# Performance work log

Hardware: AMD Instinct MI355X
Metric: run time of the kernel (lower is better)

Reference implementation:

```python
import jax, jax.numpy as jnp
import numpy as np

NUM_HEADING_BIN = 12
NUM_SIZE_CLUSTER = 8
BS = 524288
# KITTI-style mean box sizes (l, w, h) for 8 size clusters
G_MEAN_SIZE_ARR = np.array([
    [3.88, 1.63, 1.53], [0.84, 0.66, 1.76], [1.76, 0.60, 1.74], [16.17, 2.58, 3.23],
    [3.90, 1.60, 1.56], [1.73, 0.58, 1.37], [0.91, 0.48, 1.78], [2.06, 1.86, 1.66]],
    dtype=np.float32)


def setup_inputs() -> dict:
    key = jax.random.key(0)
    ks = jax.random.split(key, 13)
    f = lambda k, s: jax.random.normal(k, s, dtype=jnp.float32)
    return {
        "center": f(ks[0], (BS, 3)),
        "center_label": f(ks[1], (BS, 3)),
        "stage1_center": f(ks[2], (BS, 3)),
        "heading_scores": f(ks[3], (BS, 12)),
        "heading_residuals_normalized": f(ks[4], (BS, 12)),
        "heading_residuals": f(ks[5], (BS, 12)),
        "heading_class_label": jax.random.randint(ks[6], (BS,), 0, 12, dtype=jnp.int64),
        "heading_residuals_label": f(ks[7], (BS,)),
        "size_scores": f(ks[8], (BS, 8)),
        "size_residuals_normalized": f(ks[9], (BS, 8, 3)),
        "size_residuals": f(ks[10], (BS, 8, 3)),
        "size_class_label": jax.random.randint(ks[11], (BS,), 0, 8, dtype=jnp.int64),
        "size_residuals_label": f(ks[12], (BS, 3)),
    }


def _huber(err, delta):
    a = jnp.abs(err)
    q = jnp.minimum(a, delta)
    return jnp.mean(0.5 * q * q + delta * (a - q))


_SX = jnp.array([1, 1, -1, -1, 1, 1, -1, -1], dtype=jnp.float32)
_SY = jnp.array([1, 1, 1, 1, -1, -1, -1, -1], dtype=jnp.float32)
_SZ = jnp.array([1, -1, -1, 1, 1, -1, -1, 1], dtype=jnp.float32)


def _corners3d(centers, headings, sizes):
    # centers (bs,3), headings (bs,), sizes (bs,3) [l,w,h] -> (bs,8,3)
    l, w, h = sizes[:, 0:1], sizes[:, 1:2], sizes[:, 2:3]
    x = 0.5 * l * _SX  # (bs,8)
    y = 0.5 * h * _SY
    z = 0.5 * w * _SZ
    c = jnp.cos(headings)[:, None]
    s = jnp.sin(headings)[:, None]
    xr = c * x + s * z   # rotation about y-axis
    zr = -s * x + c * z
    return jnp.stack([xr, y, zr], axis=-1) + centers[:, None, :]


def reference(center, center_label, stage1_center, heading_scores,
              heading_residuals_normalized, heading_residuals, heading_class_label,
              heading_residuals_label, size_scores, size_residuals_normalized,
              size_residuals, size_class_label, size_residuals_label):
    corner_loss_weight, box_loss_weight = 10.0, 1.0
    mean_sizes = jnp.asarray(G_MEAN_SIZE_ARR)  # (8,3)
    hcls = heading_class_label.astype(jnp.int32)
    scls = size_class_label.astype(jnp.int32)

    center_loss = _huber(jnp.linalg.norm(center - center_label, axis=1), 2.0)
    stage1_center_loss = _huber(jnp.linalg.norm(center - stage1_center, axis=1), 1.0)

    h_logp = jax.nn.log_softmax(heading_scores, axis=1)
    heading_class_loss = -jnp.mean(jnp.take_along_axis(h_logp, hcls[:, None], axis=1))
    s_logp = jax.nn.log_softmax(size_scores, axis=1)
    size_class_loss = -jnp.mean(jnp.take_along_axis(s_logp, scls[:, None], axis=1))

    # heading residual loss (one-hot sum == gather at class index)
    hres_label_norm = heading_residuals_label / (np.pi / NUM_HEADING_BIN)
    hres_pred = jnp.take_along_axis(heading_residuals_normalized, hcls[:, None], axis=1)[:, 0]
    heading_res_loss = _huber(hres_pred - hres_label_norm, 1.0)

    # size residual loss
    sres_pred = jnp.take_along_axis(size_residuals_normalized, scls[:, None, None], axis=1)[:, 0]  # (bs,3)
    mean_size_label = mean_sizes[scls]  # (bs,3)
    sres_label_norm = size_residuals_label / mean_size_label
    size_res_loss = _huber(jnp.linalg.norm(sres_label_norm - sres_pred, axis=1), 1.0)

    # corner loss: gt_mask one-hot sum over (NH,NS) grid == gather (hcls, scls) box
    bin_centers = jnp.arange(NUM_HEADING_BIN, dtype=jnp.float32) * (2.0 * np.pi / NUM_HEADING_BIN)
    heading_pred = jnp.take_along_axis(heading_residuals, hcls[:, None], axis=1)[:, 0] + bin_centers[hcls]
    size_pred = mean_size_label + jnp.take_along_axis(size_residuals, scls[:, None, None], axis=1)[:, 0]
    corners_pred = _corners3d(center, heading_pred, size_pred)  # (bs,8,3)

    heading_label = heading_residuals_label + bin_centers[hcls]
    size_label = mean_size_label + size_residuals_label
    corners_gt = _corners3d(center_label, heading_label, size_label)
    corners_gt_flip = _corners3d(center_label, heading_label + np.pi, size_label)
    corners_dist = jnp.minimum(jnp.linalg.norm(corners_pred - corners_gt, axis=-1),
                               jnp.linalg.norm(corners_pred - corners_gt_flip, axis=-1))
    corners_loss = _huber(corners_dist, 1.0)

    total_loss = box_loss_weight * (center_loss + heading_class_loss + size_class_loss
                                    + heading_res_loss * 20.0 + size_res_loss * 20.0
                                    + stage1_center_loss + corner_loss_weight * corners_loss)
    return total_loss
```

## Files before the change

### kernel.cpp

```cpp
#include <hip/hip_runtime.h>
#include <math.h>


constexpr int BS_N  = 524288;
constexpr int NBLK  = 2048;

__constant__ float G_MEAN[8][3] = {
    {3.88f, 1.63f, 1.53f}, {0.84f, 0.66f, 1.76f}, {1.76f, 0.60f, 1.74f},
    {16.17f, 2.58f, 3.23f}, {3.90f, 1.60f, 1.56f}, {1.73f, 0.58f, 1.37f},
    {0.91f, 0.48f, 1.78f}, {2.06f, 1.86f, 1.66f}
};

__device__ __forceinline__ float huber_pos(float a, float delta) {
    return (a <= delta) ? 0.5f * a * a : delta * (a - 0.5f * delta);
}
__device__ __forceinline__ float huber_norm2(float d2, float delta) {
    return (d2 <= delta * delta) ? 0.5f * d2
                                 : delta * (sqrtf(d2) - 0.5f * delta);
}

__global__ __launch_bounds__(256) void bbox_partial(
    const float* __restrict__ center,
    const float* __restrict__ center_label,
    const float* __restrict__ stage1_center,
    const float* __restrict__ heading_scores,
    const float* __restrict__ hrn,
    const float* __restrict__ hres,
    const int*   __restrict__ hcls_in,
    const float* __restrict__ hres_label,
    const float* __restrict__ size_scores,
    const float* __restrict__ srn,
    const float* __restrict__ sres,
    const int*   __restrict__ scls_in,
    const float* __restrict__ sres_label,
    float* __restrict__ block_out)
{
    const int i = blockIdx.x * 256 + threadIdx.x;

    float contrib = 0.0f;

    const int h = hcls_in[i];
    const int s = scls_in[i];

    const float cx = center[3*i+0], cy = center[3*i+1], cz = center[3*i+2];
    const float lx = center_label[3*i+0], ly = center_label[3*i+1], lz = center_label[3*i+2];

    const float dx0 = cx - lx, dy0 = cy - ly, dz0 = cz - lz;
    contrib += huber_norm2(dx0*dx0 + dy0*dy0 + dz0*dz0, 2.0f);
    {
        const float ax = cx - stage1_center[3*i+0];
        const float ay = cy - stage1_center[3*i+1];
        const float az = cz - stage1_center[3*i+2];
        contrib += huber_norm2(ax*ax + ay*ay + az*az, 1.0f);
    }

    {
        const float4* p = reinterpret_cast<const float4*>(heading_scores + 12*i);
        const float4 a = p[0], b = p[1], c4 = p[2];
        float m = fmaxf(fmaxf(fmaxf(a.x,a.y),fmaxf(a.z,a.w)),
                  fmaxf(fmaxf(fmaxf(b.x,b.y),fmaxf(b.z,b.w)),
                        fmaxf(fmaxf(c4.x,c4.y),fmaxf(c4.z,c4.w))));
        float se = __expf(a.x-m)+__expf(a.y-m)+__expf(a.z-m)+__expf(a.w-m)
                 + __expf(b.x-m)+__expf(b.y-m)+__expf(b.z-m)+__expf(b.w-m)
                 + __expf(c4.x-m)+__expf(c4.y-m)+__expf(c4.z-m)+__expf(c4.w-m);
        const float lse = m + __logf(se);
        contrib += lse - heading_scores[12*i + h];
    }

    {
        const float4* p = reinterpret_cast<const float4*>(size_scores + 8*i);
        const float4 a = p[0], b = p[1];
        float m = fmaxf(fmaxf(fmaxf(a.x,a.y),fmaxf(a.z,a.w)),
                        fmaxf(fmaxf(b.x,b.y),fmaxf(b.z,b.w)));
        float se = __expf(a.x-m)+__expf(a.y-m)+__expf(a.z-m)+__expf(a.w-m)
                 + __expf(b.x-m)+__expf(b.y-m)+__expf(b.z-m)+__expf(b.w-m);
        const float lse = m + __logf(se);
        contrib += lse - size_scores[8*i + s];
    }

    const float hrl = hres_label[i];

    {
        const float pred = hrn[12*i + h];
        const float labn = hrl * (float)(12.0 / M_PI);
        contrib += 20.0f * huber_pos(fabsf(pred - labn), 1.0f);
    }

    const float m0 = G_MEAN[s][0], m1 = G_MEAN[s][1], m2c = G_MEAN[s][2];
    const int   sb = (8*i + s) * 3;
    const float sl0 = sres_label[3*i+0], sl1 = sres_label[3*i+1], sl2 = sres_label[3*i+2];
    {
        const float e0 = sl0 / m0 - srn[sb+0];
        const float e1 = sl1 / m1 - srn[sb+1];
        const float e2 = sl2 / m2c - srn[sb+2];
        contrib += 20.0f * huber_norm2(e0*e0 + e1*e1 + e2*e2, 1.0f);
    }

    {
        const float binc = (float)h * (float)(M_PI / 6.0);
        const float hp = hres[12*i + h] + binc;
        const float hg = hrl + binc;
        const float lp2 = 0.5f * (m0 + sres[sb+0]);
        const float wp2 = 0.5f * (m1 + sres[sb+1]);
        const float hp2 = 0.5f * (m2c + sres[sb+2]);
        const float lg2 = 0.5f * (m0 + sl0);
        const float wg2 = 0.5f * (m1 + sl1);
        const float hg2 = 0.5f * (m2c + sl2);
        float cp, sp, cg, sg;
        __sincosf(hp, &sp, &cp);
        __sincosf(hg, &sg, &cg);
        const float dyh = hp2 - hg2;

        constexpr float SX[8] = {1,1,-1,-1,1,1,-1,-1};
        constexpr float SY[8] = {1,1,1,1,-1,-1,-1,-1};
        constexpr float SZ[8] = {1,-1,-1,1,1,-1,-1,1};
        float csum = 0.0f;
        #pragma unroll
        for (int j = 0; j < 8; ++j) {
            const float axp = SX[j]*lp2, azp = SZ[j]*wp2;
            const float xrp = cp*axp + sp*azp;
            const float zrp = cp*azp - sp*axp;
            const float axg = SX[j]*lg2, azg = SZ[j]*wg2;
            const float xrg = cg*axg + sg*azg;
            const float zrg = cg*azg - sg*axg;
            const float ddy = dy0 + SY[j]*dyh;
            const float u = dx0 + xrp, v = dz0 + zrp;
            const float du1 = u - xrg, dv1 = v - zrg;
            const float du2 = u + xrg, dv2 = v + zrg;
            const float y2 = ddy*ddy;
            const float dgt = du1*du1 + y2 + dv1*dv1;
            const float dfl = du2*du2 + y2 + dv2*dv2;
            const float mm = fminf(dgt, dfl);
            csum += (mm <= 1.0f) ? 0.5f*mm : sqrtf(mm) - 0.5f;
        }
        contrib += 1.25f * csum;
    }

    #pragma unroll
    for (int off = 32; off > 0; off >>= 1)
        contrib += __shfl_down(contrib, off, 64);

    __shared__ float sdata[4];
    const int lane = threadIdx.x & 63;
    const int wid  = threadIdx.x >> 6;
    if (lane == 0) sdata[wid] = contrib;
    __syncthreads();
    if (threadIdx.x == 0)
        block_out[blockIdx.x] = (sdata[0] + sdata[1]) + (sdata[2] + sdata[3]);
}

__global__ __launch_bounds__(256) void bbox_final(
    const float* __restrict__ block_in, float* __restrict__ out)
{
    float ssum = 0.0f;
    for (int i = threadIdx.x; i < NBLK; i += 256)
        ssum += block_in[i];
    #pragma unroll
    for (int off = 32; off > 0; off >>= 1)
        ssum += __shfl_down(ssum, off, 64);

    __shared__ float sdata[4];
    const int lane = threadIdx.x & 63;
    const int wid  = threadIdx.x >> 6;
    if (lane == 0) sdata[wid] = ssum;
    __syncthreads();
    if (threadIdx.x == 0)
        out[0] = ((sdata[0] + sdata[1]) + (sdata[2] + sdata[3])) * (1.0f / (float)BS_N);
}

extern "C" void kernel_launch(void* const* d_in, const int* in_sizes, int n_in,
                              void* d_out, int out_size, void* d_ws, size_t ws_size,
                              hipStream_t stream) {
    const float* center        = (const float*)d_in[0];
    const float* center_label  = (const float*)d_in[1];
    const float* stage1_center = (const float*)d_in[2];
    const float* heading_sc    = (const float*)d_in[3];
    const float* hrn           = (const float*)d_in[4];
    const float* hres          = (const float*)d_in[5];
    const int*   hcls          = (const int*)d_in[6];
    const float* hres_label    = (const float*)d_in[7];
    const float* size_sc       = (const float*)d_in[8];
    const float* srn           = (const float*)d_in[9];
    const float* sres          = (const float*)d_in[10];
    const int*   scls          = (const int*)d_in[11];
    const float* sres_label    = (const float*)d_in[12];

    float* ws  = (float*)d_ws;
    float* out = (float*)d_out;

    bbox_partial<<<NBLK, 256, 0, stream>>>(
        center, center_label, stage1_center, heading_sc, hrn, hres,
        hcls, hres_label, size_sc, srn, sres, scls, sres_label, ws);
    bbox_final<<<1, 256, 0, stream>>>(ws, out);
}
```

Measured before the change: 40.39 us.

## Process two samples per thread with vectorized loads and register-selected scores

Each thread now handles two consecutive samples, loading indices, centers and labels as int2/float2 and the score rows as float4 vectors, which halves the grid to 1024 blocks. The label score is picked from registers with select chains instead of a second global load, and the size-residual division is replaced by multiplication with a constant reciprocal table. This is meant to cut the number of memory instructions and improve coalescing, at the cost of more registers per thread and possibly lower occupancy for latency hiding.

```diff
diff --git a/kernel.cpp b/kernel.cpp
--- a/kernel.cpp
+++ b/kernel.cpp
@@ -2,14 +2,20 @@
 #include <math.h>
 
 
-constexpr int BS_N  = 524288;
-constexpr int NBLK  = 2048;
+constexpr int BS_N = 524288;
+constexpr int NBLK = 1024;
 
 __constant__ float G_MEAN[8][3] = {
     {3.88f, 1.63f, 1.53f}, {0.84f, 0.66f, 1.76f}, {1.76f, 0.60f, 1.74f},
     {16.17f, 2.58f, 3.23f}, {3.90f, 1.60f, 1.56f}, {1.73f, 0.58f, 1.37f},
     {0.91f, 0.48f, 1.78f}, {2.06f, 1.86f, 1.66f}
 };
+__constant__ float G_RCP[8][3] = {
+    {1.0f/3.88f, 1.0f/1.63f, 1.0f/1.53f}, {1.0f/0.84f, 1.0f/0.66f, 1.0f/1.76f},
+    {1.0f/1.76f, 1.0f/0.60f, 1.0f/1.74f}, {1.0f/16.17f, 1.0f/2.58f, 1.0f/3.23f},
+    {1.0f/3.90f, 1.0f/1.60f, 1.0f/1.56f}, {1.0f/1.73f, 1.0f/0.58f, 1.0f/1.37f},
+    {1.0f/0.91f, 1.0f/0.48f, 1.0f/1.78f}, {1.0f/2.06f, 1.0f/1.86f, 1.0f/1.66f}
+};
 
 __device__ __forceinline__ float huber_pos(float a, float delta) {
     return (a <= delta) ? 0.5f * a * a : delta * (a - 0.5f * delta);
@@ -18,91 +24,81 @@
     return (d2 <= delta * delta) ? 0.5f * d2
                                  : delta * (sqrtf(d2) - 0.5f * delta);
 }
-
-__global__ __launch_bounds__(256) void bbox_partial(
-    const float* __restrict__ center,
-    const float* __restrict__ center_label,
-    const float* __restrict__ stage1_center,
-    const float* __restrict__ heading_scores,
-    const float* __restrict__ hrn,
-    const float* __restrict__ hres,
-    const int*   __restrict__ hcls_in,
-    const float* __restrict__ hres_label,
-    const float* __restrict__ size_scores,
-    const float* __restrict__ srn,
-    const float* __restrict__ sres,
-    const int*   __restrict__ scls_in,
-    const float* __restrict__ sres_label,
-    float* __restrict__ block_out)
+__device__ __forceinline__ float sel4(float4 v, int k) {
+    float r = v.x;
+    r = (k == 1) ? v.y : r;
+    r = (k == 2) ? v.z : r;
+    r = (k == 3) ? v.w : r;
+    return r;
+}
+__device__ __forceinline__ float sel12(float4 a, float4 b, float4 c, int k) {
+    float r = sel4(a, k);
+    r = (k >= 4) ? sel4(b, k - 4) : r;
+    r = (k >= 8) ? sel4(c, k - 8) : r;
+    return r;
+}
+__device__ __forceinline__ float sel8(float4 a, float4 b, int k) {
+    float r = sel4(a, k);
+    r = (k >= 4) ? sel4(b, k - 4) : r;
+    return r;
+}
+
+__device__ __forceinline__ float sample_loss(
+    int h, int s,
+    float cx, float cy, float cz,
+    float lx, float ly, float lz,
+    float tx, float ty, float tz,
+    float4 hsA, float4 hsB, float4 hsC,
+    float4 ssA, float4 ssB,
+    float hrl,
+    float hrnv, float hrev,
+    float sl0, float sl1, float sl2,
+    float sn0, float sn1, float sn2,
+    float sr0, float sr1, float sr2)
 {
-    const int i = blockIdx.x * 256 + threadIdx.x;
-
     float contrib = 0.0f;
-
-    const int h = hcls_in[i];
-    const int s = scls_in[i];
-
-    const float cx = center[3*i+0], cy = center[3*i+1], cz = center[3*i+2];
-    const float lx = center_label[3*i+0], ly = center_label[3*i+1], lz = center_label[3*i+2];
 
     const float dx0 = cx - lx, dy0 = cy - ly, dz0 = cz - lz;
     contrib += huber_norm2(dx0*dx0 + dy0*dy0 + dz0*dz0, 2.0f);
     {
-        const float ax = cx - stage1_center[3*i+0];
-        const float ay = cy - stage1_center[3*i+1];
-        const float az = cz - stage1_center[3*i+2];
+        const float ax = cx - tx, ay = cy - ty, az = cz - tz;
         contrib += huber_norm2(ax*ax + ay*ay + az*az, 1.0f);
     }
 
     {
-        const float4* p = reinterpret_cast<const float4*>(heading_scores + 12*i);
-        const float4 a = p[0], b = p[1], c4 = p[2];
-        float m = fmaxf(fmaxf(fmaxf(a.x,a.y),fmaxf(a.z,a.w)),
-                  fmaxf(fmaxf(fmaxf(b.x,b.y),fmaxf(b.z,b.w)),
-                        fmaxf(fmaxf(c4.x,c4.y),fmaxf(c4.z,c4.w))));
-        float se = __expf(a.x-m)+__expf(a.y-m)+__expf(a.z-m)+__expf(a.w-m)
-                 + __expf(b.x-m)+__expf(b.y-m)+__expf(b.z-m)+__expf(b.w-m)
-                 + __expf(c4.x-m)+__expf(c4.y-m)+__expf(c4.z-m)+__expf(c4.w-m);
-        const float lse = m + __logf(se);
-        contrib += lse - heading_scores[12*i + h];
-    }
-
-    {
-        const float4* p = reinterpret_cast<const float4*>(size_scores + 8*i);
-        const float4 a = p[0], b = p[1];
-        float m = fmaxf(fmaxf(fmaxf(a.x,a.y),fmaxf(a.z,a.w)),
-                        fmaxf(fmaxf(b.x,b.y),fmaxf(b.z,b.w)));
-        float se = __expf(a.x-m)+__expf(a.y-m)+__expf(a.z-m)+__expf(a.w-m)
-                 + __expf(b.x-m)+__expf(b.y-m)+__expf(b.z-m)+__expf(b.w-m);
-        const float lse = m + __logf(se);
-        contrib += lse - size_scores[8*i + s];
-    }
-
-    const float hrl = hres_label[i];
-
-    {
-        const float pred = hrn[12*i + h];
-        const float labn = hrl * (float)(12.0 / M_PI);
-        contrib += 20.0f * huber_pos(fabsf(pred - labn), 1.0f);
-    }
+        float m = fmaxf(fmaxf(fmaxf(hsA.x,hsA.y),fmaxf(hsA.z,hsA.w)),
+                  fmaxf(fmaxf(fmaxf(hsB.x,hsB.y),fmaxf(hsB.z,hsB.w)),
+                        fmaxf(fmaxf(hsC.x,hsC.y),fmaxf(hsC.z,hsC.w))));
+        float se = __expf(hsA.x-m)+__expf(hsA.y-m)+__expf(hsA.z-m)+__expf(hsA.w-m)
+                 + __expf(hsB.x-m)+__expf(hsB.y-m)+__expf(hsB.z-m)+__expf(hsB.w-m)
+                 + __expf(hsC.x-m)+__expf(hsC.y-m)+__expf(hsC.z-m)+__expf(hsC.w-m);
+        contrib += m + __logf(se) - sel12(hsA, hsB, hsC, h);
+    }
+    {
+        float m = fmaxf(fmaxf(fmaxf(ssA.x,ssA.y),fmaxf(ssA.z,ssA.w)),
+                        fmaxf(fmaxf(ssB.x,ssB.y),fmaxf(ssB.z,ssB.w)));
+        float se = __expf(ssA.x-m)+__expf(ssA.y-m)+__expf(ssA.z-m)+__expf(ssA.w-m)
+                 + __expf(ssB.x-m)+__expf(ssB.y-m)+__expf(ssB.z-m)+__expf(ssB.w-m);
+        contrib += m + __logf(se) - sel8(ssA, ssB, s);
+    }
+
+    contrib += 20.0f * huber_pos(fabsf(hrnv - hrl * (float)(12.0 / M_PI)), 1.0f);
 
     const float m0 = G_MEAN[s][0], m1 = G_MEAN[s][1], m2c = G_MEAN[s][2];
-    const int   sb = (8*i + s) * 3;
-    const float sl0 = sres_label[3*i+0], sl1 = sres_label[3*i+1], sl2 = sres_label[3*i+2];
-    {
-        const float e0 = sl0 / m0 - srn[sb+0];
-        const float e1 = sl1 / m1 - srn[sb+1];
-        const float e2 = sl2 / m2c - srn[sb+2];
+    {
+        const float e0 = sl0 * G_RCP[s][0] - sn0;
+        const float e1 = sl1 * G_RCP[s][1] - sn1;
+        const float e2 = sl2 * G_RCP[s][2] - sn2;
         contrib += 20.0f * huber_norm2(e0*e0 + e1*e1 + e2*e2, 1.0f);
     }
 
     {
         const float binc = (float)h * (float)(M_PI / 6.0);
-        const float hp = hres[12*i + h] + binc;
+        const float hp = hrev + binc;
         const float hg = hrl + binc;
-        const float lp2 = 0.5f * (m0 + sres[sb+0]);
-        const float wp2 = 0.5f * (m1 + sres[sb+1]);
-        const float hp2 = 0.5f * (m2c + sres[sb+2]);
+        const float lp2 = 0.5f * (m0 + sr0);
+        const float wp2 = 0.5f * (m1 + sr1);
+        const float hp2 = 0.5f * (m2c + sr2);
         const float lg2 = 0.5f * (m0 + sl0);
         const float wg2 = 0.5f * (m1 + sl1);
         const float hg2 = 0.5f * (m2c + sl2);
@@ -135,6 +131,70 @@
         }
         contrib += 1.25f * csum;
     }
+    return contrib;
+}
+
+__global__ __launch_bounds__(256) void bbox_partial(
+    const float* __restrict__ center,
+    const float* __restrict__ center_label,
+    const float* __restrict__ stage1_center,
+    const float* __restrict__ heading_scores,
+    const float* __restrict__ hrn,
+    const float* __restrict__ hres,
+    const int*   __restrict__ hcls_in,
+    const float* __restrict__ hres_label,
+    const float* __restrict__ size_scores,
+    const float* __restrict__ srn,
+    const float* __restrict__ sres,
+    const int*   __restrict__ scls_in,
+    const float* __restrict__ sres_label,
+    float* __restrict__ block_out)
+{
+    const int t  = blockIdx.x * 256 + threadIdx.x;
+    const int i0 = 2 * t;
+
+    const int2 h2 = *reinterpret_cast<const int2*>(hcls_in + i0);
+    const int2 s2 = *reinterpret_cast<const int2*>(scls_in + i0);
+
+    const float2* cp2 = reinterpret_cast<const float2*>(center        + 3*i0);
+    const float2* lp2 = reinterpret_cast<const float2*>(center_label  + 3*i0);
+    const float2* tp2 = reinterpret_cast<const float2*>(stage1_center + 3*i0);
+    const float2* rp2 = reinterpret_cast<const float2*>(sres_label    + 3*i0);
+    const float2 cA = cp2[0], cB = cp2[1], cC = cp2[2];
+    const float2 lA = lp2[0], lB = lp2[1], lC = lp2[2];
+    const float2 tA = tp2[0], tB = tp2[1], tC = tp2[2];
+    const float2 rA = rp2[0], rB = rp2[1], rC = rp2[2];
+    const float2 hl = *reinterpret_cast<const float2*>(hres_label + i0);
+
+    const float4* hsp = reinterpret_cast<const float4*>(heading_scores + 12*i0);
+    const float4 hsA0 = hsp[0], hsB0 = hsp[1], hsC0 = hsp[2];
+    const float4 hsA1 = hsp[3], hsB1 = hsp[4], hsC1 = hsp[5];
+    const float4* ssp = reinterpret_cast<const float4*>(size_scores + 8*i0);
+    const float4 ssA0 = ssp[0], ssB0 = ssp[1];
+    const float4 ssA1 = ssp[2], ssB1 = ssp[3];
+
+    const int h0 = h2.x, h1 = h2.y, s0 = s2.x, s1 = s2.y;
+    const float hrn0 = hrn [12*i0 + h0],      hrn1 = hrn [12*i0 + 12 + h1];
+    const float hre0 = hres[12*i0 + h0],      hre1 = hres[12*i0 + 12 + h1];
+    const int sb0 = (8*i0 + s0) * 3,          sb1 = (8*i0 + 8 + s1) * 3;
+    const float sn00 = srn [sb0+0], sn01 = srn [sb0+1], sn02 = srn [sb0+2];
+    const float sn10 = srn [sb1+0], sn11 = srn [sb1+1], sn12 = srn [sb1+2];
+    const float sr00 = sres[sb0+0], sr01 = sres[sb0+1], sr02 = sres[sb0+2];
+    const float sr10 = sres[sb1+0], sr11 = sres[sb1+1], sr12 = sres[sb1+2];
+
+    float contrib =
+        sample_loss(h0, s0,
+                    cA.x, cA.y, cB.x,  lA.x, lA.y, lB.x,  tA.x, tA.y, tB.x,
+                    hsA0, hsB0, hsC0,  ssA0, ssB0,
+                    hl.x, hrn0, hre0,
+                    rA.x, rA.y, rB.x,
+                    sn00, sn01, sn02,  sr00, sr01, sr02)
+      + sample_loss(h1, s1,
+                    cB.y, cC.x, cC.y,  lB.y, lC.x, lC.y,  tB.y, tC.x, tC.y,
+                    hsA1, hsB1, hsC1,  ssA1, ssB1,
+                    hl.y, hrn1, hre1,
+                    rB.y, rC.x, rC.y,
+                    sn10, sn11, sn12,  sr10, sr11, sr12);
 
     #pragma unroll
     for (int off = 32; off > 0; off >>= 1)
```

Result: no change. 41.14 us (+1.9%).
